# Kernel optimization log

Hardware: AMD Instinct MI355X
Metric: run time of the kernel (lower is better)

Reference implementation:

```python
import jax, jax.numpy as jnp
import numpy as np

B, S, HID = 2, 1024, 2048
H, KV, D = 32, 8, 64          # heads, kv heads, head_dim
G = H // KV                    # GQA groups
THETA = 10000.0


def _rope_cos_sin(seq_len):
    # (S, D/2) cos/sin tables, interleaved-pair RoPE
    freqs = 1.0 / THETA ** (jnp.arange(0, D, 2, dtype=jnp.float32) / D)
    t = jnp.arange(seq_len, dtype=jnp.float32)
    f = jnp.outer(t, freqs)
    return jnp.cos(f), jnp.sin(f)


def _apply_rope(x, cos, sin):
    # x: (B, S, h, D); cos/sin: (S, D/2) -> broadcast (1, S, 1, D/2)
    c = cos[None, :, None, :]
    s = sin[None, :, None, :]
    xe, xo = x[..., ::2], x[..., 1::2]
    oe = xe * c - xo * s
    oo = xo * c + xe * s
    # re-interleave even/odd
    return jnp.stack([oe, oo], axis=-1).reshape(x.shape)


def setup_inputs() -> dict:
    key = jax.random.key(0)
    ks = jax.random.split(key, 5)
    return {
        "hidden_states": jax.random.normal(ks[0], (B, S, HID), jnp.float32),
        "Wq": jax.random.normal(ks[1], (HID, H * D), jnp.float32) * 0.02,
        "Wk": jax.random.normal(ks[2], (HID, KV * D), jnp.float32) * 0.02,
        "Wv": jax.random.normal(ks[3], (HID, KV * D), jnp.float32) * 0.02,
        "Wo": jax.random.normal(ks[4], (H * D, HID), jnp.float32) * 0.02,
    }


def reference(hidden_states, Wq, Wk, Wv, Wo):
    b, s, _ = hidden_states.shape
    q = (hidden_states @ Wq).reshape(b, s, H, D)
    k = (hidden_states @ Wk).reshape(b, s, KV, D)
    v = (hidden_states @ Wv).reshape(b, s, KV, D)

    cos, sin = _rope_cos_sin(s)
    q = _apply_rope(q, cos, sin)
    k = _apply_rope(k, cos, sin)

    # GQA: repeat kv heads to match query heads
    k = jnp.repeat(k, G, axis=2)  # (b, s, H, D)
    v = jnp.repeat(v, G, axis=2)

    scale = jnp.sqrt(jnp.float32(D))
    scores = jnp.einsum("bqhd,bkhd->bhqk", q, k) / scale  # (b, H, s, s)
    causal = jnp.tril(jnp.ones((s, s), jnp.float32))[None, None]
    scores = jnp.where(causal < 0.5, jnp.float32(-1e10), scores)
    weights = jax.nn.softmax(scores, axis=-1)
    ctx = jnp.einsum("bhqk,bkhd->bqhd", weights, v).reshape(b, s, H * D)
    return ctx @ Wo
```

## Files before the change

kernel.cpp:

```cpp
#include <hip/hip_runtime.h>
#include <hip/hip_bf16.h>

typedef __attribute__((ext_vector_type(8))) __bf16 bf16x8;
typedef __attribute__((ext_vector_type(4))) float f32x4;

#define MFMA16(a,b,c) __builtin_amdgcn_mfma_f32_16x16x32_bf16(a,b,c,0,0,0)

__device__ __forceinline__ unsigned short f2b(float x){
  __hip_bfloat16 h = __float2bfloat16(x);
  return __builtin_bit_cast(unsigned short, h);
}

__device__ __forceinline__ void gload16(const unsigned short* g, unsigned short* l){
  __builtin_amdgcn_global_load_lds(
      (const __attribute__((address_space(1))) unsigned int*)g,
      (__attribute__((address_space(3))) unsigned int*)l, 16, 0, 0);
}

__global__ __launch_bounds__(256) void k_prep(
    const float* __restrict__ X,  const float* __restrict__ Wq,
    const float* __restrict__ Wk, const float* __restrict__ Wv,
    const float* __restrict__ Wo,
    float* __restrict__ ct, float* __restrict__ st,
    unsigned short* __restrict__ Xb, unsigned short* __restrict__ Wt,
    unsigned short* __restrict__ Wot)
{
  __shared__ float t[32][33];
  int bid = blockIdx.x;
  if (bid < 128){
    int i = bid*256 + threadIdx.x;
    int tt = i >> 5, f = i & 31;
    float freq = powf(10000.0f, -(float)f/32.0f);
    float a = (float)tt * freq;
    ct[i] = cosf(a); st[i] = sinf(a);
    return;
  }
  bid -= 128;
  if (bid < 1024){
    const int n4 = 2048*2048/4;
    for (int i = bid*256 + threadIdx.x; i < n4; i += 1024*256){
      float4 v = ((const float4*)X)[i];
      ushort4 o; o.x=f2b(v.x); o.y=f2b(v.y); o.z=f2b(v.z); o.w=f2b(v.w);
      ((ushort4*)Xb)[i] = o;
    }
    return;
  }
  bid -= 1024;
  if (bid < 6144){
    int bx = bid % 96, by = bid / 96;
    int n0 = bx*32, k0 = by*32;
    const float* src; int N, nl;
    if (n0 < 2048)      { src=Wq; N=2048; nl=n0; }
    else if (n0 < 2560) { src=Wk; N=512;  nl=n0-2048; }
    else                { src=Wv; N=512;  nl=n0-2560; }
    int r = threadIdx.x>>5, c = threadIdx.x&31;
    #pragma unroll
    for (int it=0; it<4; ++it)
      t[r+8*it][c] = src[(size_t)(k0+r+8*it)*N + nl + c];
    __syncthreads();
    #pragma unroll
    for (int it=0; it<4; ++it)
      Wt[(size_t)(n0+r+8*it)*2048 + k0 + c] = f2b(t[c][r+8*it]);
    return;
  }
  bid -= 6144;
  {
    int n0 = (bid & 63)*32, k0 = (bid >> 6)*32;
    int r = threadIdx.x>>5, c = threadIdx.x&31;
    #pragma unroll
    for (int it=0; it<4; ++it)
      t[r+8*it][c] = Wo[(size_t)(k0+r+8*it)*2048 + n0 + c];
    __syncthreads();
    #pragma unroll
    for (int it=0; it<4; ++it)
      Wot[(size_t)(n0+r+8*it)*2048 + k0 + c] = f2b(t[c][r+8*it]);
  }
}

__global__ __launch_bounds__(256) void k_qkv(
    const unsigned short* __restrict__ A, const unsigned short* __restrict__ Bt,
    const float* __restrict__ ct, const float* __restrict__ st,
    unsigned short* __restrict__ qb, unsigned short* __restrict__ kb,
    unsigned short* __restrict__ vt)
{
  __shared__ unsigned short As[3][128*32];
  __shared__ unsigned short Bs[3][64*32];
  const int xcd = blockIdx.x & 7, idx = blockIdx.x >> 3;
  const int mt = idx & 15;
  const int nt = xcd*6 + (idx >> 4);
  const int bm = mt*128, bn_g = nt*64;
  const int tid=threadIdx.x, wave=tid>>6, lane=tid&63;
  const int lrow=lane&15, kgrp=lane>>4;
  const int wm=(wave>>1)*64, wn=(wave&1)*32;
  const int arow = tid>>2;
  const int acs  = (((tid&3) ^ ((tid>>3)&3)))*8;
  const int ksw  = (kgrp ^ ((lrow>>1)&3))*8;
  f32x4 acc[4][2] = {};

  #define STAGE_Q(buf, k0) do {                                                               \
    gload16(&A [(size_t)(bm + arow     )*2048 + (k0) + acs], &As[buf][(wave*64)*8]);          \
    gload16(&A [(size_t)(bm + 64 + arow)*2048 + (k0) + acs], &As[buf][(256 + wave*64)*8]);    \
    gload16(&Bt[(size_t)(bn_g + arow   )*2048 + (k0) + acs], &Bs[buf][(wave*64)*8]);          \
  } while(0)

  #define COMPUTE_Q(buf) do {                                          \
    bf16x8 a0,a1,a2,a3,b0,b1;                                          \
    a0 = *(const bf16x8*)&As[buf][(wm+ 0+lrow)*32 + ksw];              \
    a1 = *(const bf16x8*)&As[buf][(wm+16+lrow)*32 + ksw];              \
    a2 = *(const bf16x8*)&As[buf][(wm+32+lrow)*32 + ksw];              \
    a3 = *(const bf16x8*)&As[buf][(wm+48+lrow)*32 + ksw];              \
    b0 = *(const bf16x8*)&Bs[buf][(wn+ 0+lrow)*32 + ksw];              \
    b1 = *(const bf16x8*)&Bs[buf][(wn+16+lrow)*32 + ksw];              \
    acc[0][0]=MFMA16(a0,b0,acc[0][0]); acc[0][1]=MFMA16(a0,b1,acc[0][1]); \
    acc[1][0]=MFMA16(a1,b0,acc[1][0]); acc[1][1]=MFMA16(a1,b1,acc[1][1]); \
    acc[2][0]=MFMA16(a2,b0,acc[2][0]); acc[2][1]=MFMA16(a2,b1,acc[2][1]); \
    acc[3][0]=MFMA16(a3,b0,acc[3][0]); acc[3][1]=MFMA16(a3,b1,acc[3][1]); \
  } while(0)

  STAGE_Q(0, 0);
  STAGE_Q(1, 32);
  int cur = 0;
  #pragma unroll 1
  for (int t=0; t<64; ++t){
    asm volatile("s_waitcnt vmcnt(3)" ::: "memory");
    __builtin_amdgcn_s_barrier();
    int kn = t+2; if (kn > 63) kn = 63;
    int nb = cur+2; if (nb > 2) nb -= 3;
    STAGE_Q(nb, kn*32);
    COMPUTE_Q(cur);
    cur = (cur==2) ? 0 : cur+1;
  }

  const int wtype = (bn_g < 2048) ? 0 : (bn_g < 2560 ? 1 : 2);
  const float qscale = 0.125f * 1.44269504f;
  #pragma unroll
  for (int mi=0;mi<4;mi++){
    #pragma unroll
    for (int ni=0;ni<2;ni++){
      int gr0 = bm + wm + mi*16 + kgrp*4;
      int gc  = bn_g + wn + ni*16 + lrow;
      if (wtype==2){
        int c = gc - 2560;
        int bq = gr0 >> 10, s0 = gr0 & 1023;
        ushort4 o;
        o.x=f2b(acc[mi][ni][0]); o.y=f2b(acc[mi][ni][1]);
        o.z=f2b(acc[mi][ni][2]); o.w=f2b(acc[mi][ni][3]);
        *(ushort4*)&vt[((size_t)(bq*512 + c))*1024 + s0] = o;
      } else {
        int d = gc & 63, fi = d >> 1, odd = d & 1;
        #pragma unroll
        for (int r=0;r<4;r++){
          float x = acc[mi][ni][r];
          float p = __shfl_xor(x, 1, 64);
          int srow = (gr0 + r) & 1023;
          float c = ct[srow*32 + fi], sn = st[srow*32 + fi];
          float o = odd ? (x*c + p*sn) : (x*c - p*sn);
          if (wtype==0) qb[(size_t)(gr0+r)*2048 + gc] = f2b(o*qscale);
          else          kb[(size_t)(gr0+r)*512 + (gc-2048)] = f2b(o);
        }
      }
    }
  }
  #undef STAGE_Q
  #undef COMPUTE_Q
}

#define LDP 72
__global__ __launch_bounds__(256) void k_attn(
    const unsigned short* __restrict__ qb, const unsigned short* __restrict__ kb,
    const unsigned short* __restrict__ vt, unsigned short* __restrict__ ctxb)
{
  __shared__ unsigned short Ks[2][64*LDP];
  __shared__ unsigned short Vs[2][64*LDP];
  __shared__ unsigned short QP[64*LDP];

  const int kvh = blockIdx.x & 7;
  const int s   = blockIdx.x >> 3;
  const int b   = s >> 5;
  const int hh  = (s >> 3) & 3;
  const int p   = s & 7;
  const int h   = kvh*4 + hh;

  const int tid=threadIdx.x, wave=tid>>6, lane=tid&63;
  const int lrow=lane&15, kgrp=lane>>4;
  const int wq = wave*16;
  const int sr = tid>>2, seg = (tid&3)*16;

  const unsigned short* kbase = kb + (size_t)(b*1024)*512 + kvh*64 + seg;
  const unsigned short* vbase = vt + ((size_t)(b*512 + kvh*64 + sr))*1024 + seg;

  #pragma unroll
  for (int phase=0; phase<2; ++phase){
    const int qt = phase==0 ? 15-p : p;
    const int q0 = qt*64;

    __syncthreads();
    {
      const unsigned short* src = qb + (size_t)(b*1024 + q0 + sr)*2048 + h*64 + seg;
      *(uint4*)&QP[sr*LDP + seg]     = *(const uint4*)&src[0];
      *(uint4*)&QP[sr*LDP + seg + 8] = *(const uint4*)&src[8];
      const unsigned short* ksrc = kbase + (size_t)sr*512;
      *(uint4*)&Ks[0][sr*LDP + seg]     = *(const uint4*)&ksrc[0];
      *(uint4*)&Ks[0][sr*LDP + seg + 8] = *(const uint4*)&ksrc[8];
      *(uint4*)&Vs[0][sr*LDP + seg]     = *(const uint4*)&vbase[0];
      *(uint4*)&Vs[0][sr*LDP + seg + 8] = *(const uint4*)&vbase[8];
    }
    __syncthreads();

    bf16x8 qa[2];
    #pragma unroll
    for (int ks=0;ks<2;ks++)
      qa[ks] = *(const bf16x8*)&QP[(wq+lrow)*LDP + ks*32 + kgrp*8];

    float m_run = -1e30f, l_run = 0.f;
    f32x4 out[4] = {};

    for (int j=0;j<=qt;j++){
      const int cb = j&1;
      uint4 kra, krb, vra, vrb;
      if (j < qt){
        const unsigned short* ksrc = kbase + (size_t)((j+1)*64 + sr)*512;
        kra = *(const uint4*)&ksrc[0]; krb = *(const uint4*)&ksrc[8];
        const unsigned short* vsrc = vbase + (j+1)*64;
        vra = *(const uint4*)&vsrc[0]; vrb = *(const uint4*)&vsrc[8];
      }

      f32x4 sc[4] = {};
      __builtin_amdgcn_s_setprio(1);
      #pragma unroll
      for (int ks=0;ks<2;ks++){
        #pragma unroll
        for (int ni=0;ni<4;ni++){
          bf16x8 kf = *(const bf16x8*)&Ks[cb][(ni*16+lrow)*LDP + ks*32 + kgrp*8];
          sc[ni] = MFMA16(kf, qa[ks], sc[ni]);
        }
      }
      __builtin_amdgcn_s_setprio(0);

      if (j == qt){
        #pragma unroll
        for (int ni=0;ni<4;ni++)
          #pragma unroll
          for (int r=0;r<4;r++)
            if (ni*16 + kgrp*4 + r > wq + lrow) sc[ni][r] = -1e30f;
      }

      float mx = sc[0][0];
      #pragma unroll
      for (int ni=0;ni<4;ni++)
        #pragma unroll
        for (int r=0;r<4;r++) mx = fmaxf(mx, sc[ni][r]);
      mx = fmaxf(mx, __shfl_xor(mx, 16, 64));
      mx = fmaxf(mx, __shfl_xor(mx, 32, 64));
      if (__any(mx > m_run + 12.0f)){
        float mnew = fmaxf(m_run, mx);
        float corr = exp2f(m_run - mnew);
        m_run = mnew;
        l_run *= corr;
        #pragma unroll
        for (int di=0;di<4;di++)
          #pragma unroll
          for (int r=0;r<4;r++) out[di][r] *= corr;
      }
      float rsum = 0.f;
      #pragma unroll
      for (int ni=0;ni<4;ni++)
        #pragma unroll
        for (int r=0;r<4;r++){
          float pv = exp2f(sc[ni][r] - m_run);
          sc[ni][r] = pv;
          rsum += pv;
        }
      rsum += __shfl_xor(rsum, 16, 64);
      rsum += __shfl_xor(rsum, 32, 64);
      l_run += rsum;

      #pragma unroll
      for (int ni=0;ni<4;ni++){
        ushort4 o;
        o.x=f2b(sc[ni][0]); o.y=f2b(sc[ni][1]);
        o.z=f2b(sc[ni][2]); o.w=f2b(sc[ni][3]);
        *(ushort4*)&QP[(wq+lrow)*LDP + ni*16 + kgrp*4] = o;
      }

      __builtin_amdgcn_s_setprio(1);
      #pragma unroll
      for (int ks2=0;ks2<2;ks2++){
        bf16x8 pb = *(const bf16x8*)&QP[(wq+lrow)*LDP + ks2*32 + kgrp*8];
        #pragma unroll
        for (int di=0;di<4;di++){
          bf16x8 vf = *(const bf16x8*)&Vs[cb][(di*16+lrow)*LDP + ks2*32 + kgrp*8];
          out[di] = MFMA16(vf, pb, out[di]);
        }
      }
      __builtin_amdgcn_s_setprio(0);

      if (j < qt){
        const int nb = (j+1)&1;
        *(uint4*)&Ks[nb][sr*LDP + seg]     = kra;
        *(uint4*)&Ks[nb][sr*LDP + seg + 8] = krb;
        *(uint4*)&Vs[nb][sr*LDP + seg]     = vra;
        *(uint4*)&Vs[nb][sr*LDP + seg + 8] = vrb;
      }
      __syncthreads();
    }

    float rl = 1.0f / l_run;
    #pragma unroll
    for (int di=0;di<4;di++){
      ushort4 o;
      o.x=f2b(out[di][0]*rl); o.y=f2b(out[di][1]*rl);
      o.z=f2b(out[di][2]*rl); o.w=f2b(out[di][3]*rl);
      *(ushort4*)&ctxb[(size_t)(b*1024 + q0 + wq + lrow)*2048
                       + h*64 + di*16 + kgrp*4] = o;
    }
  }
}

__global__ __launch_bounds__(256) void k_oproj(
    const unsigned short* __restrict__ A, const unsigned short* __restrict__ Bt,
    float* __restrict__ out)
{
  __shared__ unsigned short As[3][128*32];
  __shared__ unsigned short Bs[3][64*32];
  const int xcd = blockIdx.x & 7, idx = blockIdx.x >> 3;
  const int mt = idx & 15;
  const int nt = xcd*4 + (idx >> 4);
  const int bm = mt*128, bn = nt*64;
  const int tid=threadIdx.x, wave=tid>>6, lane=tid&63;
  const int lrow=lane&15, kgrp=lane>>4;
  const int wm=(wave>>1)*64, wn=(wave&1)*32;
  const int arow = tid>>2;
  const int acs  = (((tid&3) ^ ((tid>>3)&3)))*8;
  const int ksw  = (kgrp ^ ((lrow>>1)&3))*8;
  f32x4 acc[4][2] = {};

  #define STAGE_O(buf, k0) do {                                                               \
    gload16(&A [(size_t)(bm + arow     )*2048 + (k0) + acs], &As[buf][(wave*64)*8]);          \
    gload16(&A [(size_t)(bm + 64 + arow)*2048 + (k0) + acs], &As[buf][(256 + wave*64)*8]);    \
    gload16(&Bt[(size_t)(bn + arow     )*2048 + (k0) + acs], &Bs[buf][(wave*64)*8]);          \
  } while(0)

  #define COMPUTE_O(buf) do {                                          \
    bf16x8 a0,a1,a2,a3,b0,b1;                                          \
    a0 = *(const bf16x8*)&As[buf][(wm+ 0+lrow)*32 + ksw];              \
    a1 = *(const bf16x8*)&As[buf][(wm+16+lrow)*32 + ksw];              \
    a2 = *(const bf16x8*)&As[buf][(wm+32+lrow)*32 + ksw];              \
    a3 = *(const bf16x8*)&As[buf][(wm+48+lrow)*32 + ksw];              \
    b0 = *(const bf16x8*)&Bs[buf][(wn+ 0+lrow)*32 + ksw];              \
    b1 = *(const bf16x8*)&Bs[buf][(wn+16+lrow)*32 + ksw];              \
    acc[0][0]=MFMA16(a0,b0,acc[0][0]); acc[0][1]=MFMA16(a0,b1,acc[0][1]); \
    acc[1][0]=MFMA16(a1,b0,acc[1][0]); acc[1][1]=MFMA16(a1,b1,acc[1][1]); \
    acc[2][0]=MFMA16(a2,b0,acc[2][0]); acc[2][1]=MFMA16(a2,b1,acc[2][1]); \
    acc[3][0]=MFMA16(a3,b0,acc[3][0]); acc[3][1]=MFMA16(a3,b1,acc[3][1]); \
  } while(0)

  STAGE_O(0, 0);
  STAGE_O(1, 32);
  int cur = 0;
  #pragma unroll 1
  for (int t=0; t<64; ++t){
    asm volatile("s_waitcnt vmcnt(3)" ::: "memory");
    __builtin_amdgcn_s_barrier();
    int kn = t+2; if (kn > 63) kn = 63;
    int nb = cur+2; if (nb > 2) nb -= 3;
    STAGE_O(nb, kn*32);
    COMPUTE_O(cur);
    cur = (cur==2) ? 0 : cur+1;
  }

  #pragma unroll
  for (int mi=0;mi<4;mi++)
    #pragma unroll
    for (int ni=0;ni<2;ni++){
      int gr0 = bm + wm + mi*16 + kgrp*4;
      int gc  = bn + wn + ni*16 + lrow;
      #pragma unroll
      for (int r=0;r<4;r++)
        out[(size_t)(gr0+r)*2048 + gc] = acc[mi][ni][r];
    }
  #undef STAGE_O
  #undef COMPUTE_O
}

extern "C" void kernel_launch(void* const* d_in, const int* in_sizes, int n_in,
                              void* d_out, int out_size, void* d_ws, size_t ws_size,
                              hipStream_t stream)
{
  const float* X  = (const float*)d_in[0];
  const float* Wq = (const float*)d_in[1];
  const float* Wk = (const float*)d_in[2];
  const float* Wv = (const float*)d_in[3];
  const float* Wo = (const float*)d_in[4];
  float* out = (float*)d_out;
  char* ws = (char*)d_ws;

  const size_t MB = 1048576;
  float* ct = (float*)ws;
  float* st = (float*)(ws + 128*1024);
  unsigned short* Xb   = (unsigned short*)(ws + 256*1024);
  unsigned short* Wt   = (unsigned short*)(ws + 256*1024 + 8*MB);
  unsigned short* Wot  = (unsigned short*)(ws + 256*1024 + 20*MB);
  unsigned short* qb   = (unsigned short*)(ws + 256*1024 + 28*MB);
  unsigned short* kb   = (unsigned short*)(ws + 256*1024 + 36*MB);
  unsigned short* vt   = (unsigned short*)(ws + 256*1024 + 38*MB);
  unsigned short* ctxb = (unsigned short*)(ws + 256*1024 + 40*MB);

  hipLaunchKernelGGL(k_prep, dim3(11392), dim3(256), 0, stream,
                     X, Wq, Wk, Wv, Wo, ct, st, Xb, Wt, Wot);
  hipLaunchKernelGGL(k_qkv, dim3(768), dim3(256), 0, stream,
                     Xb, Wt, ct, st, qb, kb, vt);
  hipLaunchKernelGGL(k_attn, dim3(512), dim3(256), 0, stream, qb, kb, vt, ctxb);
  hipLaunchKernelGGL(k_oproj, dim3(512), dim3(256), 0, stream, ctxb, Wot, out);
}
```

Before: 132.2 us.

## Switch QKV and O-proj GEMMs to BK=64 double-buffered pipeline

Both GEMM kernels move from a K-step of 32 with a three-stage LDS ring to a K-step of 64 with two buffers. This halves the number of barriers and loop iterations, and a new 8-way XOR swizzle matches the wider 64-element rows. The cost is that each loop now waits for all outstanding loads (vmcnt(0)) before its barrier, so only one stage of prefetch overlaps compute instead of two. LDS use per block rises from 36KB to 48KB.

```diff
diff --git a/kernel.cpp b/kernel.cpp
--- a/kernel.cpp
+++ b/kernel.cpp
@@ -83,8 +83,8 @@
     unsigned short* __restrict__ qb, unsigned short* __restrict__ kb,
     unsigned short* __restrict__ vt)
 {
-  __shared__ unsigned short As[3][128*32];
-  __shared__ unsigned short Bs[3][64*32];
+  __shared__ unsigned short As[2][128*64];
+  __shared__ unsigned short Bs[2][64*64];
   const int xcd = blockIdx.x & 7, idx = blockIdx.x >> 3;
   const int mt = idx & 15;
   const int nt = xcd*6 + (idx >> 4);
@@ -92,25 +92,28 @@
   const int tid=threadIdx.x, wave=tid>>6, lane=tid&63;
   const int lrow=lane&15, kgrp=lane>>4;
   const int wm=(wave>>1)*64, wn=(wave&1)*32;
-  const int arow = tid>>2;
-  const int acs  = (((tid&3) ^ ((tid>>3)&3)))*8;
-  const int ksw  = (kgrp ^ ((lrow>>1)&3))*8;
+  const int rowb = tid>>3;
+  const int csl  = ((tid&7) ^ (rowb&7))*8;
+  const int rdo  = (kgrp ^ (lrow&7))*8;
   f32x4 acc[4][2] = {};
 
-  #define STAGE_Q(buf, k0) do {                                                               \
-    gload16(&A [(size_t)(bm + arow     )*2048 + (k0) + acs], &As[buf][(wave*64)*8]);          \
-    gload16(&A [(size_t)(bm + 64 + arow)*2048 + (k0) + acs], &As[buf][(256 + wave*64)*8]);    \
-    gload16(&Bt[(size_t)(bn_g + arow   )*2048 + (k0) + acs], &Bs[buf][(wave*64)*8]);          \
+  #define STAGE_Q(buf, k0) do {                                                                 \
+    gload16(&A [(size_t)(bm + rowb     )*2048 + (k0) + csl], &As[buf][(wave*64)*8]);            \
+    gload16(&A [(size_t)(bm + 32 + rowb)*2048 + (k0) + csl], &As[buf][(256 + wave*64)*8]);      \
+    gload16(&A [(size_t)(bm + 64 + rowb)*2048 + (k0) + csl], &As[buf][(512 + wave*64)*8]);      \
+    gload16(&A [(size_t)(bm + 96 + rowb)*2048 + (k0) + csl], &As[buf][(768 + wave*64)*8]);      \
+    gload16(&Bt[(size_t)(bn_g + rowb   )*2048 + (k0) + csl], &Bs[buf][(wave*64)*8]);            \
+    gload16(&Bt[(size_t)(bn_g+32+ rowb )*2048 + (k0) + csl], &Bs[buf][(256 + wave*64)*8]);      \
   } while(0)
 
-  #define COMPUTE_Q(buf) do {                                          \
+  #define HALF_Q(buf, xo) do {                                         \
     bf16x8 a0,a1,a2,a3,b0,b1;                                          \
-    a0 = *(const bf16x8*)&As[buf][(wm+ 0+lrow)*32 + ksw];              \
-    a1 = *(const bf16x8*)&As[buf][(wm+16+lrow)*32 + ksw];              \
-    a2 = *(const bf16x8*)&As[buf][(wm+32+lrow)*32 + ksw];              \
-    a3 = *(const bf16x8*)&As[buf][(wm+48+lrow)*32 + ksw];              \
-    b0 = *(const bf16x8*)&Bs[buf][(wn+ 0+lrow)*32 + ksw];              \
-    b1 = *(const bf16x8*)&Bs[buf][(wn+16+lrow)*32 + ksw];              \
+    a0 = *(const bf16x8*)&As[buf][(wm+ 0+lrow)*64 + (rdo^(xo))];       \
+    a1 = *(const bf16x8*)&As[buf][(wm+16+lrow)*64 + (rdo^(xo))];       \
+    a2 = *(const bf16x8*)&As[buf][(wm+32+lrow)*64 + (rdo^(xo))];       \
+    a3 = *(const bf16x8*)&As[buf][(wm+48+lrow)*64 + (rdo^(xo))];       \
+    b0 = *(const bf16x8*)&Bs[buf][(wn+ 0+lrow)*64 + (rdo^(xo))];       \
+    b1 = *(const bf16x8*)&Bs[buf][(wn+16+lrow)*64 + (rdo^(xo))];       \
     acc[0][0]=MFMA16(a0,b0,acc[0][0]); acc[0][1]=MFMA16(a0,b1,acc[0][1]); \
     acc[1][0]=MFMA16(a1,b0,acc[1][0]); acc[1][1]=MFMA16(a1,b1,acc[1][1]); \
     acc[2][0]=MFMA16(a2,b0,acc[2][0]); acc[2][1]=MFMA16(a2,b1,acc[2][1]); \
@@ -118,17 +121,16 @@
   } while(0)
 
   STAGE_Q(0, 0);
-  STAGE_Q(1, 32);
-  int cur = 0;
+  asm volatile("s_waitcnt vmcnt(0)" ::: "memory");
+  __builtin_amdgcn_s_barrier();
   #pragma unroll 1
-  for (int t=0; t<64; ++t){
-    asm volatile("s_waitcnt vmcnt(3)" ::: "memory");
+  for (int t=0; t<32; ++t){
+    int kn = t+1; if (kn > 31) kn = 31;
+    STAGE_Q((t&1)^1, kn*64);
+    HALF_Q(t&1, 0);
+    HALF_Q(t&1, 32);
+    asm volatile("s_waitcnt vmcnt(0)" ::: "memory");
     __builtin_amdgcn_s_barrier();
-    int kn = t+2; if (kn > 63) kn = 63;
-    int nb = cur+2; if (nb > 2) nb -= 3;
-    STAGE_Q(nb, kn*32);
-    COMPUTE_Q(cur);
-    cur = (cur==2) ? 0 : cur+1;
   }
 
   const int wtype = (bn_g < 2048) ? 0 : (bn_g < 2560 ? 1 : 2);
@@ -162,7 +164,7 @@
     }
   }
   #undef STAGE_Q
-  #undef COMPUTE_Q
+  #undef HALF_Q
 }
 
 #define LDP 72
@@ -321,8 +323,8 @@
     const unsigned short* __restrict__ A, const unsigned short* __restrict__ Bt,
     float* __restrict__ out)
 {
-  __shared__ unsigned short As[3][128*32];
-  __shared__ unsigned short Bs[3][64*32];
+  __shared__ unsigned short As[2][128*64];
+  __shared__ unsigned short Bs[2][64*64];
   const int xcd = blockIdx.x & 7, idx = blockIdx.x >> 3;
   const int mt = idx & 15;
   const int nt = xcd*4 + (idx >> 4);
@@ -330,25 +332,28 @@
   const int tid=threadIdx.x, wave=tid>>6, lane=tid&63;
   const int lrow=lane&15, kgrp=lane>>4;
   const int wm=(wave>>1)*64, wn=(wave&1)*32;
-  const int arow = tid>>2;
-  const int acs  = (((tid&3) ^ ((tid>>3)&3)))*8;
-  const int ksw  = (kgrp ^ ((lrow>>1)&3))*8;
+  const int rowb = tid>>3;
+  const int csl  = ((tid&7) ^ (rowb&7))*8;
+  const int rdo  = (kgrp ^ (lrow&7))*8;
   f32x4 acc[4][2] = {};
 
-  #define STAGE_O(buf, k0) do {                                                               \
-    gload16(&A [(size_t)(bm + arow     )*2048 + (k0) + acs], &As[buf][(wave*64)*8]);          \
-    gload16(&A [(size_t)(bm + 64 + arow)*2048 + (k0) + acs], &As[buf][(256 + wave*64)*8]);    \
-    gload16(&Bt[(size_t)(bn + arow     )*2048 + (k0) + acs], &Bs[buf][(wave*64)*8]);          \
+  #define STAGE_O(buf, k0) do {                                                                 \
+    gload16(&A [(size_t)(bm + rowb     )*2048 + (k0) + csl], &As[buf][(wave*64)*8]);            \
+    gload16(&A [(size_t)(bm + 32 + rowb)*2048 + (k0) + csl], &As[buf][(256 + wave*64)*8]);      \
+    gload16(&A [(size_t)(bm + 64 + rowb)*2048 + (k0) + csl], &As[buf][(512 + wave*64)*8]);      \
+    gload16(&A [(size_t)(bm + 96 + rowb)*2048 + (k0) + csl], &As[buf][(768 + wave*64)*8]);      \
+    gload16(&Bt[(size_t)(bn + rowb     )*2048 + (k0) + csl], &Bs[buf][(wave*64)*8]);            \
+    gload16(&Bt[(size_t)(bn + 32 + rowb)*2048 + (k0) + csl], &Bs[buf][(256 + wave*64)*8]);      \
   } while(0)
 
-  #define COMPUTE_O(buf) do {                                          \
+  #define HALF_O(buf, xo) do {                                         \
     bf16x8 a0,a1,a2,a3,b0,b1;                                          \
-    a0 = *(const bf16x8*)&As[buf][(wm+ 0+lrow)*32 + ksw];              \
-    a1 = *(const bf16x8*)&As[buf][(wm+16+lrow)*32 + ksw];              \
-    a2 = *(const bf16x8*)&As[buf][(wm+32+lrow)*32 + ksw];              \
-    a3 = *(const bf16x8*)&As[buf][(wm+48+lrow)*32 + ksw];              \
-    b0 = *(const bf16x8*)&Bs[buf][(wn+ 0+lrow)*32 + ksw];              \
-    b1 = *(const bf16x8*)&Bs[buf][(wn+16+lrow)*32 + ksw];              \
+    a0 = *(const bf16x8*)&As[buf][(wm+ 0+lrow)*64 + (rdo^(xo))];       \
+    a1 = *(const bf16x8*)&As[buf][(wm+16+lrow)*64 + (rdo^(xo))];       \
+    a2 = *(const bf16x8*)&As[buf][(wm+32+lrow)*64 + (rdo^(xo))];       \
+    a3 = *(const bf16x8*)&As[buf][(wm+48+lrow)*64 + (rdo^(xo))];       \
+    b0 = *(const bf16x8*)&Bs[buf][(wn+ 0+lrow)*64 + (rdo^(xo))];       \
+    b1 = *(const bf16x8*)&Bs[buf][(wn+16+lrow)*64 + (rdo^(xo))];       \
     acc[0][0]=MFMA16(a0,b0,acc[0][0]); acc[0][1]=MFMA16(a0,b1,acc[0][1]); \
     acc[1][0]=MFMA16(a1,b0,acc[1][0]); acc[1][1]=MFMA16(a1,b1,acc[1][1]); \
     acc[2][0]=MFMA16(a2,b0,acc[2][0]); acc[2][1]=MFMA16(a2,b1,acc[2][1]); \
@@ -356,17 +361,16 @@
   } while(0)
 
   STAGE_O(0, 0);
-  STAGE_O(1, 32);
-  int cur = 0;
+  asm volatile("s_waitcnt vmcnt(0)" ::: "memory");
+  __builtin_amdgcn_s_barrier();
   #pragma unroll 1
-  for (int t=0; t<64; ++t){
-    asm volatile("s_waitcnt vmcnt(3)" ::: "memory");
+  for (int t=0; t<32; ++t){
+    int kn = t+1; if (kn > 31) kn = 31;
+    STAGE_O((t&1)^1, kn*64);
+    HALF_O(t&1, 0);
+    HALF_O(t&1, 32);
+    asm volatile("s_waitcnt vmcnt(0)" ::: "memory");
     __builtin_amdgcn_s_barrier();
-    int kn = t+2; if (kn > 63) kn = 63;
-    int nb = cur+2; if (nb > 2) nb -= 3;
-    STAGE_O(nb, kn*32);
-    COMPUTE_O(cur);
-    cur = (cur==2) ? 0 : cur+1;
   }
 
   #pragma unroll
@@ -380,7 +384,7 @@
         out[(size_t)(gr0+r)*2048 + gc] = acc[mi][ni][r];
     }
   #undef STAGE_O
-  #undef COMPUTE_O
+  #undef HALF_O
 }
 
 extern "C" void kernel_launch(void* const* d_in, const int* in_sizes, int n_in,
```

Result: slower. 135.9 us (+2.8%).

## Process both causal query tiles in one KV loop sharing K/V tiles

Applied to the files above, without the earlier changes.

The attention kernel previously handled its two paired query tiles (15-p and p) in two sequential phases, each streaming K/V tiles from global memory. Now both Q tiles are loaded up front and a single loop over KV tiles updates two independent online-softmax states, with the short tile active only for j <= p. Each K/V tile is therefore fetched and staged in LDS once, and one prologue and its barrier disappear. In exchange, register pressure rises from a second set of accumulators and Q fragments, which may reduce occupancy.

```diff
diff --git a/kernel.cpp b/kernel.cpp
--- a/kernel.cpp
+++ b/kernel.cpp
@@ -180,6 +180,8 @@
   const int hh  = (s >> 3) & 3;
   const int p   = s & 7;
   const int h   = kvh*4 + hh;
+  const int qtA = 15-p, qtB = p;
+  const int q0A = qtA*64, q0B = qtB*64;
 
   const int tid=threadIdx.x, wave=tid>>6, lane=tid&63;
   const int lrow=lane&15, kgrp=lane>>4;
@@ -189,42 +191,47 @@
   const unsigned short* kbase = kb + (size_t)(b*1024)*512 + kvh*64 + seg;
   const unsigned short* vbase = vt + ((size_t)(b*512 + kvh*64 + sr))*1024 + seg;
 
+  bf16x8 qaA[2], qaB[2];
+  {
+    const unsigned short* src = qb + (size_t)(b*1024 + q0A + sr)*2048 + h*64 + seg;
+    *(uint4*)&QP[sr*LDP + seg]     = *(const uint4*)&src[0];
+    *(uint4*)&QP[sr*LDP + seg + 8] = *(const uint4*)&src[8];
+  }
   #pragma unroll
-  for (int phase=0; phase<2; ++phase){
-    const int qt = phase==0 ? 15-p : p;
-    const int q0 = qt*64;
-
-    __syncthreads();
+  for (int ks=0;ks<2;ks++)
+    qaA[ks] = *(const bf16x8*)&QP[(wq+lrow)*LDP + ks*32 + kgrp*8];
+  {
+    const unsigned short* src = qb + (size_t)(b*1024 + q0B + sr)*2048 + h*64 + seg;
+    *(uint4*)&QP[sr*LDP + seg]     = *(const uint4*)&src[0];
+    *(uint4*)&QP[sr*LDP + seg + 8] = *(const uint4*)&src[8];
+  }
+  #pragma unroll
+  for (int ks=0;ks<2;ks++)
+    qaB[ks] = *(const bf16x8*)&QP[(wq+lrow)*LDP + ks*32 + kgrp*8];
+
+  {
+    const unsigned short* ksrc = kbase + (size_t)sr*512;
+    *(uint4*)&Ks[0][sr*LDP + seg]     = *(const uint4*)&ksrc[0];
+    *(uint4*)&Ks[0][sr*LDP + seg + 8] = *(const uint4*)&ksrc[8];
+    *(uint4*)&Vs[0][sr*LDP + seg]     = *(const uint4*)&vbase[0];
+    *(uint4*)&Vs[0][sr*LDP + seg + 8] = *(const uint4*)&vbase[8];
+  }
+  __syncthreads();
+
+  float mA = -1e30f, lA = 0.f, mB = -1e30f, lB = 0.f;
+  f32x4 outA[4] = {}, outB[4] = {};
+
+  for (int j=0;j<=qtA;j++){
+    const int cb = j&1;
+    uint4 kra, krb, vra, vrb;
+    if (j < qtA){
+      const unsigned short* ksrc = kbase + (size_t)((j+1)*64 + sr)*512;
+      kra = *(const uint4*)&ksrc[0]; krb = *(const uint4*)&ksrc[8];
+      const unsigned short* vsrc = vbase + (j+1)*64;
+      vra = *(const uint4*)&vsrc[0]; vrb = *(const uint4*)&vsrc[8];
+    }
+
     {
-      const unsigned short* src = qb + (size_t)(b*1024 + q0 + sr)*2048 + h*64 + seg;
-      *(uint4*)&QP[sr*LDP + seg]     = *(const uint4*)&src[0];
-      *(uint4*)&QP[sr*LDP + seg + 8] = *(const uint4*)&src[8];
-      const unsigned short* ksrc = kbase + (size_t)sr*512;
-      *(uint4*)&Ks[0][sr*LDP + seg]     = *(const uint4*)&ksrc[0];
-      *(uint4*)&Ks[0][sr*LDP + seg + 8] = *(const uint4*)&ksrc[8];
-      *(uint4*)&Vs[0][sr*LDP + seg]     = *(const uint4*)&vbase[0];
-      *(uint4*)&Vs[0][sr*LDP + seg + 8] = *(const uint4*)&vbase[8];
-    }
-    __syncthreads();
-
-    bf16x8 qa[2];
-    #pragma unroll
-    for (int ks=0;ks<2;ks++)
-      qa[ks] = *(const bf16x8*)&QP[(wq+lrow)*LDP + ks*32 + kgrp*8];
-
-    float m_run = -1e30f, l_run = 0.f;
-    f32x4 out[4] = {};
-
-    for (int j=0;j<=qt;j++){
-      const int cb = j&1;
-      uint4 kra, krb, vra, vrb;
-      if (j < qt){
-        const unsigned short* ksrc = kbase + (size_t)((j+1)*64 + sr)*512;
-        kra = *(const uint4*)&ksrc[0]; krb = *(const uint4*)&ksrc[8];
-        const unsigned short* vsrc = vbase + (j+1)*64;
-        vra = *(const uint4*)&vsrc[0]; vrb = *(const uint4*)&vsrc[8];
-      }
-
       f32x4 sc[4] = {};
       __builtin_amdgcn_s_setprio(1);
       #pragma unroll
@@ -232,12 +239,12 @@
         #pragma unroll
         for (int ni=0;ni<4;ni++){
           bf16x8 kf = *(const bf16x8*)&Ks[cb][(ni*16+lrow)*LDP + ks*32 + kgrp*8];
-          sc[ni] = MFMA16(kf, qa[ks], sc[ni]);
+          sc[ni] = MFMA16(kf, qaA[ks], sc[ni]);
         }
       }
       __builtin_amdgcn_s_setprio(0);
 
-      if (j == qt){
+      if (j == qtA){
         #pragma unroll
         for (int ni=0;ni<4;ni++)
           #pragma unroll
@@ -252,28 +259,26 @@
         for (int r=0;r<4;r++) mx = fmaxf(mx, sc[ni][r]);
       mx = fmaxf(mx, __shfl_xor(mx, 16, 64));
       mx = fmaxf(mx, __shfl_xor(mx, 32, 64));
-      if (__any(mx > m_run + 12.0f)){
-        float mnew = fmaxf(m_run, mx);
-        float corr = exp2f(m_run - mnew);
-        m_run = mnew;
-        l_run *= corr;
+      if (__any(mx > mA + 12.0f)){
+        float mnew = fmaxf(mA, mx);
+        float corr = exp2f(mA - mnew);
+        mA = mnew; lA *= corr;
         #pragma unroll
         for (int di=0;di<4;di++)
           #pragma unroll
-          for (int r=0;r<4;r++) out[di][r] *= corr;
+          for (int r=0;r<4;r++) outA[di][r] *= corr;
       }
       float rsum = 0.f;
       #pragma unroll
       for (int ni=0;ni<4;ni++)
         #pragma unroll
         for (int r=0;r<4;r++){
-          float pv = exp2f(sc[ni][r] - m_run);
-          sc[ni][r] = pv;
-          rsum += pv;
+          float pv = exp2f(sc[ni][r] - mA);
+          sc[ni][r] = pv; rsum += pv;
         }
       rsum += __shfl_xor(rsum, 16, 64);
       rsum += __shfl_xor(rsum, 32, 64);
-      l_run += rsum;
+      lA += rsum;
 
       #pragma unroll
       for (int ni=0;ni<4;ni++){
@@ -282,7 +287,6 @@
         o.z=f2b(sc[ni][2]); o.w=f2b(sc[ni][3]);
         *(ushort4*)&QP[(wq+lrow)*LDP + ni*16 + kgrp*4] = o;
       }
-
       __builtin_amdgcn_s_setprio(1);
       #pragma unroll
       for (int ks2=0;ks2<2;ks2++){
@@ -290,30 +294,103 @@
         #pragma unroll
         for (int di=0;di<4;di++){
           bf16x8 vf = *(const bf16x8*)&Vs[cb][(di*16+lrow)*LDP + ks2*32 + kgrp*8];
-          out[di] = MFMA16(vf, pb, out[di]);
+          outA[di] = MFMA16(vf, pb, outA[di]);
         }
       }
       __builtin_amdgcn_s_setprio(0);
-
-      if (j < qt){
-        const int nb = (j+1)&1;
-        *(uint4*)&Ks[nb][sr*LDP + seg]     = kra;
-        *(uint4*)&Ks[nb][sr*LDP + seg + 8] = krb;
-        *(uint4*)&Vs[nb][sr*LDP + seg]     = vra;
-        *(uint4*)&Vs[nb][sr*LDP + seg + 8] = vrb;
-      }
-      __syncthreads();
-    }
-
-    float rl = 1.0f / l_run;
-    #pragma unroll
-    for (int di=0;di<4;di++){
-      ushort4 o;
-      o.x=f2b(out[di][0]*rl); o.y=f2b(out[di][1]*rl);
-      o.z=f2b(out[di][2]*rl); o.w=f2b(out[di][3]*rl);
-      *(ushort4*)&ctxb[(size_t)(b*1024 + q0 + wq + lrow)*2048
-                       + h*64 + di*16 + kgrp*4] = o;
-    }
+    }
+
+    if (j <= qtB){
+      f32x4 sc[4] = {};
+      __builtin_amdgcn_s_setprio(1);
+      #pragma unroll
+      for (int ks=0;ks<2;ks++){
+        #pragma unroll
+        for (int ni=0;ni<4;ni++){
+          bf16x8 kf = *(const bf16x8*)&Ks[cb][(ni*16+lrow)*LDP + ks*32 + kgrp*8];
+          sc[ni] = MFMA16(kf, qaB[ks], sc[ni]);
+        }
+      }
+      __builtin_amdgcn_s_setprio(0);
+
+      if (j == qtB){
+        #pragma unroll
+        for (int ni=0;ni<4;ni++)
+          #pragma unroll
+          for (int r=0;r<4;r++)
+            if (ni*16 + kgrp*4 + r > wq + lrow) sc[ni][r] = -1e30f;
+      }
+
+      float mx = sc[0][0];
+      #pragma unroll
+      for (int ni=0;ni<4;ni++)
+        #pragma unroll
+        for (int r=0;r<4;r++) mx = fmaxf(mx, sc[ni][r]);
+      mx = fmaxf(mx, __shfl_xor(mx, 16, 64));
+      mx = fmaxf(mx, __shfl_xor(mx, 32, 64));
+      if (__any(mx > mB + 12.0f)){
+        float mnew = fmaxf(mB, mx);
+        float corr = exp2f(mB - mnew);
+        mB = mnew; lB *= corr;
+        #pragma unroll
+        for (int di=0;di<4;di++)
+          #pragma unroll
+          for (int r=0;r<4;r++) outB[di][r] *= corr;
+      }
+      float rsum = 0.f;
+      #pragma unroll
+      for (int ni=0;ni<4;ni++)
+        #pragma unroll
+        for (int r=0;r<4;r++){
+          float pv = exp2f(sc[ni][r] - mB);
+          sc[ni][r] = pv; rsum += pv;
+        }
+      rsum += __shfl_xor(rsum, 16, 64);
+      rsum += __shfl_xor(rsum, 32, 64);
+      lB += rsum;
+
+      #pragma unroll
+      for (int ni=0;ni<4;ni++){
+        ushort4 o;
+        o.x=f2b(sc[ni][0]); o.y=f2b(sc[ni][1]);
+        o.z=f2b(sc[ni][2]); o.w=f2b(sc[ni][3]);
+        *(ushort4*)&QP[(wq+lrow)*LDP + ni*16 + kgrp*4] = o;
+      }
+      __builtin_amdgcn_s_setprio(1);
+      #pragma unroll
+      for (int ks2=0;ks2<2;ks2++){
+        bf16x8 pb = *(const bf16x8*)&QP[(wq+lrow)*LDP + ks2*32 + kgrp*8];
+        #pragma unroll
+        for (int di=0;di<4;di++){
+          bf16x8 vf = *(const bf16x8*)&Vs[cb][(di*16+lrow)*LDP + ks2*32 + kgrp*8];
+          outB[di] = MFMA16(vf, pb, outB[di]);
+        }
+      }
+      __builtin_amdgcn_s_setprio(0);
+    }
+
+    if (j < qtA){
+      const int nb = (j+1)&1;
+      *(uint4*)&Ks[nb][sr*LDP + seg]     = kra;
+      *(uint4*)&Ks[nb][sr*LDP + seg + 8] = krb;
+      *(uint4*)&Vs[nb][sr*LDP + seg]     = vra;
+      *(uint4*)&Vs[nb][sr*LDP + seg + 8] = vrb;
+    }
+    __syncthreads();
+  }
+
+  float rlA = 1.0f / lA, rlB = 1.0f / lB;
+  #pragma unroll
+  for (int di=0;di<4;di++){
+    ushort4 oa, ob;
+    oa.x=f2b(outA[di][0]*rlA); oa.y=f2b(outA[di][1]*rlA);
+    oa.z=f2b(outA[di][2]*rlA); oa.w=f2b(outA[di][3]*rlA);
+    *(ushort4*)&ctxb[(size_t)(b*1024 + q0A + wq + lrow)*2048
+                     + h*64 + di*16 + kgrp*4] = oa;
+    ob.x=f2b(outB[di][0]*rlB); ob.y=f2b(outB[di][1]*rlB);
+    ob.z=f2b(outB[di][2]*rlB); ob.w=f2b(outB[di][3]*rlB);
+    *(ushort4*)&ctxb[(size_t)(b*1024 + q0B + wq + lrow)*2048
+                     + h*64 + di*16 + kgrp*4] = ob;
   }
 }
 
```

New measurement: 133.0 us. Within noise of the previous version (+0.6%).
